# Kernel tuning notes

Hardware: AMD Instinct MI355X
Metric: run time of the kernel (lower is better)

The kernel has to match this reference:

```python
import jax, jax.numpy as jnp
import numpy as np

D_MODEL = 1024
NUM_HEADS = 16
D_K = D_MODEL // NUM_HEADS
THETA = 10000.0
SEQ = 2048
BATCH = 2


def _rope(t, positions):
    # t: [b, h, s, d_k]; positions: [s]
    half = D_K // 2
    freqs = 1.0 / (THETA ** (jnp.arange(0, D_K, 2, dtype=jnp.float32) / D_K))  # [half]
    angles = positions.astype(jnp.float32)[:, None] * freqs[None, :]  # [s, half]
    cos = jnp.cos(angles)  # [s, half]
    sin = jnp.sin(angles)
    tr = t.reshape(t.shape[:-1] + (half, 2))  # pairs are (even, odd) interleaved
    x1, x2 = tr[..., 0], tr[..., 1]
    r1 = x1 * cos - x2 * sin
    r2 = x1 * sin + x2 * cos
    return jnp.stack([r1, r2], axis=-1).reshape(t.shape)


def setup_inputs() -> dict:
    key = jax.random.key(0)
    ks = jax.random.split(key, 5)
    std = float(np.sqrt(2.0 / (D_MODEL + D_MODEL)))
    return {
        "x": jax.random.normal(ks[0], (BATCH, SEQ, D_MODEL), dtype=jnp.float32),
        "token_positions": jnp.arange(SEQ, dtype=jnp.int64 if jax.config.jax_enable_x64 else jnp.int32),
        "wq": std * jax.random.normal(ks[1], (D_MODEL, D_MODEL), dtype=jnp.float32),
        "wk": std * jax.random.normal(ks[2], (D_MODEL, D_MODEL), dtype=jnp.float32),
        "wv": std * jax.random.normal(ks[3], (D_MODEL, D_MODEL), dtype=jnp.float32),
        "wo": std * jax.random.normal(ks[4], (D_MODEL, D_MODEL), dtype=jnp.float32),
    }


def reference(x, token_positions, wq, wk, wv, wo):
    b, s, _ = x.shape
    # projections: weight is (d_out, d_in), y = x @ W^T
    def proj(w):
        y = jnp.einsum('bsd,od->bso', x, w)
        return y.reshape(b, s, NUM_HEADS, D_K).transpose(0, 2, 1, 3)  # [b,h,s,dk]
    Q, K, V = proj(wq), proj(wk), proj(wv)
    Q = _rope(Q, token_positions)
    K = _rope(K, token_positions)
    scale = 1.0 / jnp.sqrt(jnp.asarray(D_K, dtype=x.dtype))
    scores = jnp.einsum('bhqd,bhkd->bhqk', Q, K) * scale  # [b,h,s,s]
    causal = jnp.tril(jnp.ones((s, s), dtype=bool))
    scores = jnp.where(causal, scores, jnp.asarray(-jnp.inf, dtype=scores.dtype))
    attn = jax.nn.softmax(scores, axis=-1)
    out = jnp.einsum('bhqk,bhkd->bhqd', attn, V)  # [b,h,s,dk]
    out = out.transpose(0, 2, 1, 3).reshape(b, s, D_MODEL)
    return jnp.einsum('bsd,od->bso', out, wo)
```

## Files before the change

### kernel.cpp

```cpp
#include <hip/hip_runtime.h>
#include <hip/hip_bf16.h>
#include <math.h>

#define BATCH  2
#define SEQ    2048
#define DMODEL 1024
#define NHEADS 16
#define DK     64

typedef __hip_bfloat16 bf16;
typedef short s16x8 __attribute__((ext_vector_type(8)));
typedef float f32x4 __attribute__((ext_vector_type(4)));

union P8 { int4 i4; s16x8 v; short s[8]; };

static __device__ __forceinline__ unsigned short f2bu(float f) {
    bf16 h = __float2bfloat16(f);
    return *reinterpret_cast<unsigned short*>(&h);
}

static __device__ __forceinline__ void gll16(const void* g, void* l) {
    __builtin_amdgcn_global_load_lds(
        (const __attribute__((address_space(1))) unsigned int*)g,
        (__attribute__((address_space(3))) unsigned int*)l, 16, 0, 0);
}

#define BAR()    __builtin_amdgcn_s_barrier()
#define LGKM0()  do { asm volatile("s_waitcnt lgkmcnt(0)" ::: "memory"); \
                      __builtin_amdgcn_sched_barrier(0); } while (0)
#define WVM(n)   do { asm volatile("s_waitcnt vmcnt(" #n ")" ::: "memory"); \
                      __builtin_amdgcn_sched_barrier(0); } while (0)

__global__ __launch_bounds__(256) void conv_k(
    const float* __restrict__ x, const float* __restrict__ wq,
    const float* __restrict__ wk, const float* __restrict__ wv,
    const float* __restrict__ wo, bf16* __restrict__ dst)
{
    const size_t e0 = ((size_t)blockIdx.x * 256 + threadIdx.x) << 3;
    const float* src;
    bf16* d;
    if (e0 < (size_t)4194304) { src = x + e0; d = dst + e0; }
    else {
        const size_t r = e0 - 4194304;
        const int wsel = (int)(r >> 20);
        const size_t off = r & 1048575;
        src = (wsel == 0 ? wq : wsel == 1 ? wk : wsel == 2 ? wv : wo) + off;
        d = dst + 4194304 + ((size_t)wsel << 20) + off;
    }
    const float4 a = *(const float4*)src;
    const float4 b = *(const float4*)(src + 4);
    P8 p;
    p.s[0] = (short)f2bu(a.x); p.s[1] = (short)f2bu(a.y);
    p.s[2] = (short)f2bu(a.z); p.s[3] = (short)f2bu(a.w);
    p.s[4] = (short)f2bu(b.x); p.s[5] = (short)f2bu(b.y);
    p.s[6] = (short)f2bu(b.z); p.s[7] = (short)f2bu(b.w);
    *(int4*)d = p.i4;
}

__global__ __launch_bounds__(512, 2) void gemm_qkv(
    const bf16* __restrict__ Ab, const bf16* __restrict__ Wb,
    bf16* __restrict__ O0, bf16* __restrict__ O1, bf16* __restrict__ O2)
{
    __shared__ __align__(16) short As[2][256 * 64];
    __shared__ __align__(16) short Ws[2][256 * 64];
    const int tid  = threadIdx.x;
    const int wid  = tid >> 6;
    const int lane = tid & 63;
    const int ln   = lane & 15;
    const int quad = lane >> 4;
    const int wr   = wid >> 2;
    const int wc   = wid & 3;
    const int swz  = ln & 7;

    const int orig = blockIdx.x;
    const int wg = (orig & 7) * 24 + (orig >> 3);
    const int m_base = (wg & 15) << 8;
    const int nz = wg >> 4;
    const int z  = nz >> 2;
    const int n_base = (nz & 3) << 8;
    const bf16* Wz = Wb + ((size_t)z << 20);

    const int lrw = lane >> 3;
    const int lcs = ((lane & 7) ^ lrw) << 3;

    auto stageHalf = [&](int b, int kt, int q) {
        if (kt >= 16) return;
        const int rs = (q & 1) * 128 + wid * 16;
        if (q < 2) {
            const size_t src = (size_t)(m_base + rs + lrw) * DMODEL
                             + (size_t)(kt * 64 + lcs);
            short* d = &As[b][rs * 64];
            gll16(Ab + src,              d);
            gll16(Ab + src + 8 * DMODEL, d + 8 * 64);
        } else {
            const size_t src = (size_t)(n_base + rs + lrw) * DMODEL
                             + (size_t)(kt * 64 + lcs);
            short* d = &Ws[b][rs * 64];
            gll16(Wz + src,              d);
            gll16(Wz + src + 8 * DMODEL, d + 8 * 64);
        }
    };

    const f32x4 zero4 = {0.f, 0.f, 0.f, 0.f};
    f32x4 acc[8][4];
    #pragma unroll
    for (int i = 0; i < 8; ++i)
        #pragma unroll
        for (int j = 0; j < 4; ++j) acc[i][j] = zero4;

    s16x8 af[4][2], bw01[2][2], bw23[2][2];

    auto readA = [&](const short* Sb, int mg) {
        #pragma unroll
        for (int mi = 0; mi < 4; ++mi)
            #pragma unroll
            for (int kk = 0; kk < 2; ++kk)
                af[mi][kk] = *(const s16x8*)&Sb[
                    (wr * 128 + mg * 64 + 16 * mi + ln) * 64 +
                    ((((kk << 2) + quad) ^ swz) << 3)];
    };
    auto readB = [&](const short* Sb, int np, s16x8 (&bwp)[2][2]) {
        #pragma unroll
        for (int nj = 0; nj < 2; ++nj)
            #pragma unroll
            for (int kk = 0; kk < 2; ++kk)
                bwp[nj][kk] = *(const s16x8*)&Sb[
                    (wc * 64 + np * 32 + 16 * nj + ln) * 64 +
                    ((((kk << 2) + quad) ^ swz) << 3)];
    };
    auto mmac = [&](int mg, int np, const s16x8 (&bwp)[2][2]) {
        #pragma unroll
        for (int mi = 0; mi < 4; ++mi)
            #pragma unroll
            for (int nj = 0; nj < 2; ++nj)
                #pragma unroll
                for (int kk = 0; kk < 2; ++kk)
                    acc[mg * 4 + mi][np * 2 + nj] =
                        __builtin_amdgcn_mfma_f32_16x16x32_bf16(
                            af[mi][kk], bwp[nj][kk],
                            acc[mg * 4 + mi][np * 2 + nj], 0, 0, 0);
    };

    stageHalf(0, 0, 0); stageHalf(0, 0, 1);
    stageHalf(0, 0, 2); stageHalf(0, 0, 3);
    stageHalf(1, 1, 0);
    WVM(2);
    BAR();

    #pragma unroll 1
    for (int i = 0; i < 8; ++i) {
        const int ta = 2 * i, tb = 2 * i + 1;
        readA(As[0], 0); readB(Ws[0], 0, bw01);
        stageHalf(1, tb, 1);
        BAR(); LGKM0();
        __builtin_amdgcn_s_setprio(1); mmac(0, 0, bw01);
        __builtin_amdgcn_s_setprio(0); BAR();
        readB(Ws[0], 1, bw23);
        stageHalf(1, tb, 2);
        BAR(); LGKM0();
        __builtin_amdgcn_s_setprio(1); mmac(0, 1, bw23);
        __builtin_amdgcn_s_setprio(0); BAR();
        readA(As[0], 1);
        stageHalf(1, tb, 3);
        BAR(); LGKM0();
        __builtin_amdgcn_s_setprio(1); mmac(1, 0, bw01);
        __builtin_amdgcn_s_setprio(0); BAR();
        stageHalf(0, ta + 2, 0);
        if (i < 7) { WVM(2); } else { WVM(0); }
        BAR();
        __builtin_amdgcn_s_setprio(1); mmac(1, 1, bw23);
        __builtin_amdgcn_s_setprio(0); BAR();
        readA(As[1], 0); readB(Ws[1], 0, bw01);
        stageHalf(0, ta + 2, 1);
        BAR(); LGKM0();
        __builtin_amdgcn_s_setprio(1); mmac(0, 0, bw01);
        __builtin_amdgcn_s_setprio(0); BAR();
        readB(Ws[1], 1, bw23);
        stageHalf(0, ta + 2, 2);
        BAR(); LGKM0();
        __builtin_amdgcn_s_setprio(1); mmac(0, 1, bw23);
        __builtin_amdgcn_s_setprio(0); BAR();
        readA(As[1], 1);
        stageHalf(0, ta + 2, 3);
        BAR(); LGKM0();
        __builtin_amdgcn_s_setprio(1); mmac(1, 0, bw01);
        __builtin_amdgcn_s_setprio(0); BAR();
        stageHalf(1, tb + 2, 0);
        if (i < 7) { WVM(2); } else { WVM(0); }
        BAR();
        __builtin_amdgcn_s_setprio(1); mmac(1, 1, bw23);
        __builtin_amdgcn_s_setprio(0); BAR();
    }

    if (z < 2) {
        bf16* C = (z == 0) ? O0 : O1;
        const float qs = (z == 0) ? 0.125f * 1.44269504089f : 1.0f;
        const int h = (n_base >> 6) + wc;
        const float sgn = (ln & 1) ? 1.0f : -1.0f;
        float freq[4];
        #pragma unroll
        for (int nj = 0; nj < 4; ++nj)
            freq[nj] = exp2f(-(float)((16 * nj + ln) >> 1) * 0.4152410119f);
        #pragma unroll
        for (int mi = 0; mi < 8; ++mi) {
            #pragma unroll
            for (int r = 0; r < 4; ++r) {
                const int m = m_base + wr * 128 + 16 * mi + quad * 4 + r;
                const int b = m >> 11, s = m & (SEQ - 1);
                const float fs = (float)s;
                float sn[4], cs[4];
                #pragma unroll
                for (int nj = 0; nj < 4; ++nj)
                    __sincosf(fs * freq[nj], &sn[nj], &cs[nj]);
                bf16* row = C + (((size_t)(b * NHEADS + h) * SEQ) + s) * DK;
                #pragma unroll
                for (int nj = 0; nj < 4; ++nj) {
                    const float v = acc[mi][nj][r];
                    const float p = __shfl_xor(v, 1, 64);
                    row[16 * nj + ln] =
                        __float2bfloat16((v * cs[nj] + sgn * p * sn[nj]) * qs);
                }
            }
        }
    } else {
        #pragma unroll
        for (int nj = 0; nj < 4; ++nj) {
            const int n = n_base + wc * 64 + 16 * nj + ln;
            const int h = n >> 6, d = n & (DK - 1);
            #pragma unroll
            for (int mi = 0; mi < 8; ++mi) {
                const int m0v = m_base + wr * 128 + 16 * mi + quad * 4;
                const int b = m0v >> 11, s0 = m0v & (SEQ - 1);
                ushort4 pk;
                pk.x = f2bu(acc[mi][nj][0]); pk.y = f2bu(acc[mi][nj][1]);
                pk.z = f2bu(acc[mi][nj][2]); pk.w = f2bu(acc[mi][nj][3]);
                *(ushort4*)(O2 + (((size_t)(b * NHEADS + h) * DK) + d) * SEQ + s0) = pk;
            }
        }
    }
}

__global__ __launch_bounds__(256) void gemm_wo(
    const bf16* __restrict__ Ab, const bf16* __restrict__ Wb,
    float* __restrict__ Of)
{
    __shared__ __align__(16) short As[64 * 64];
    __shared__ __align__(16) short Ws2[128 * 64];
    const int tid  = threadIdx.x;
    const int w    = tid >> 6;
    const int lane = tid & 63;
    const int ln   = lane & 15;
    const int quad = lane >> 4;
    const int id   = blockIdx.x;
    const int m_base = (id & 63) << 6;
    const int n_base = (id >> 6) << 7;

    const int lrw = lane >> 3;
    const int lcs = ((lane & 7) ^ lrw) << 3;
    const int am = m_base + 16 * w + lrw;
    short* ldsA = &As[1024 * w];
    const size_t wbase = (size_t)(n_base + 32 * w + lrw) * DMODEL + lcs;
    short* ldsW = &Ws2[2048 * w];

    const f32x4 zero4 = {0.f, 0.f, 0.f, 0.f};
    f32x4 acc[2][4];
    #pragma unroll
    for (int i = 0; i < 2; ++i)
        #pragma unroll
        for (int j = 0; j < 4; ++j) acc[i][j] = zero4;

    const int mo = (w >> 1) << 5, no = (w & 1) << 6;
    const int swz = ln & 7;

    for (int k0 = 0; k0 < DMODEL; k0 += 64) {
        const int hh = k0 >> 6;
        __syncthreads();
        #pragma unroll
        for (int t = 0; t < 2; ++t) {
            const int m = am + t * 8;
            const int b = m >> 11, s = m & (SEQ - 1);
            gll16(Ab + (((size_t)(b * NHEADS + hh) * SEQ) + s) * DK + lcs,
                  ldsA + t * 512);
        }
        #pragma unroll
        for (int t = 0; t < 4; ++t)
            gll16(Wb + wbase + (size_t)t * 8 * DMODEL + k0, ldsW + t * 512);
        __syncthreads();
        #pragma unroll
        for (int t = 0; t < 2; ++t) {
            const int co = (((t << 2) + quad) ^ swz) << 3;
            s16x8 af[2], bw[4];
            #pragma unroll
            for (int i = 0; i < 2; ++i)
                af[i] = *(const s16x8*)&As[(mo + 16 * i + ln) * 64 + co];
            #pragma unroll
            for (int j = 0; j < 4; ++j)
                bw[j] = *(const s16x8*)&Ws2[(no + 16 * j + ln) * 64 + co];
            #pragma unroll
            for (int mi = 0; mi < 2; ++mi)
                #pragma unroll
                for (int ni = 0; ni < 4; ++ni)
                    acc[mi][ni] = __builtin_amdgcn_mfma_f32_16x16x32_bf16(
                        af[mi], bw[ni], acc[mi][ni], 0, 0, 0);
        }
    }

    #pragma unroll
    for (int mi = 0; mi < 2; ++mi)
        #pragma unroll
        for (int ni = 0; ni < 4; ++ni) {
            const int n = n_base + no + 16 * ni + ln;
            #pragma unroll
            for (int r = 0; r < 4; ++r) {
                const int m = m_base + mo + 16 * mi + quad * 4 + r;
                Of[(size_t)m * DMODEL + n] = acc[mi][ni][r];
            }
        }
}

__global__ __launch_bounds__(256) void attn_k(bf16* __restrict__ Q,
                                              const bf16* __restrict__ Kg,
                                              const bf16* __restrict__ VT)
{
    __shared__ __align__(16) short Ks[64 * 64];
    __shared__ __align__(16) short Vs[64 * 64];
    __shared__ __align__(16) short PT[4 * 16 * 64];
    const int tid  = threadIdx.x;
    const int w    = tid >> 6;
    const int lane = tid & 63;
    const int ln   = lane & 15;
    const int quad = lane >> 4;
    const int bh = blockIdx.x & 31;
    const int row = blockIdx.x >> 5;
    const int bk = row & 7, bg = row >> 3;
    const int qt = (bg == 0) ? 31 - bk : (bg == 1) ? 15 - bk
                 : (bg == 2) ? 16 + bk : bk;
    const size_t base = (size_t)bh * (SEQ * DK);
    const int srow = tid >> 2;
    const int sc   = (tid & 3) << 4;
    const int qrow = qt * 64 + 16 * w + ln;

    const int sr7 = srow & 7;
    const int wofs0 = srow * 64 + ((((sc >> 3)    ) ^ sr7) << 3);
    const int wofs1 = srow * 64 + ((((sc >> 3) | 1) ^ sr7) << 3);
    const int l7 = ln & 7;
    const int rof0 = ln * 64 + ((quad ^ l7) << 3);
    const int rof1 = ln * 64 + (((4 | quad) ^ l7) << 3);
    short* PTw = &PT[w << 10];

    P8 qa0, qa1;
    {
        const bf16* qsrc = Q + base + (size_t)qrow * DK + quad * 8;
        qa0.i4 = *(const int4*)(qsrc);
        qa1.i4 = *(const int4*)(qsrc + 32);
    }
    const f32x4 zero4 = {0.f, 0.f, 0.f, 0.f};
    f32x4 o[4];
    #pragma unroll
    for (int mt = 0; mt < 4; ++mt) o[mt] = zero4;
    float lsum = 0.f;

    P8 kk[2], vv[2];
    {
        const bf16* ksrc = Kg + base + (size_t)srow * DK + sc;
        kk[0].i4 = *(const int4*)(ksrc);
        kk[1].i4 = *(const int4*)(ksrc + 8);
        const bf16* vsrc = VT + base + (size_t)srow * SEQ + sc;
        vv[0].i4 = *(const int4*)(vsrc);
        vv[1].i4 = *(const int4*)(vsrc + 8);
    }

    for (int kb = 0; kb <= qt; ++kb) {
        __syncthreads();
        *(s16x8*)&Ks[wofs0] = kk[0].v;
        *(s16x8*)&Ks[wofs1] = kk[1].v;
        *(s16x8*)&Vs[wofs0] = vv[0].v;
        *(s16x8*)&Vs[wofs1] = vv[1].v;
        __syncthreads();

        if (kb < qt) {
            const bf16* ksrc = Kg + base + (size_t)((kb + 1) * 64 + srow) * DK + sc;
            kk[0].i4 = *(const int4*)(ksrc);
            kk[1].i4 = *(const int4*)(ksrc + 8);
            const bf16* vsrc = VT + base + (size_t)srow * SEQ + (kb + 1) * 64 + sc;
            vv[0].i4 = *(const int4*)(vsrc);
            vv[1].i4 = *(const int4*)(vsrc + 8);
        }

        f32x4 sf[4];
        #pragma unroll
        for (int mt = 0; mt < 4; ++mt) {
            sf[mt] = zero4;
            s16x8 ka  = *(const s16x8*)&Ks[mt * 1024 + rof0];
            s16x8 kb2 = *(const s16x8*)&Ks[mt * 1024 + rof1];
            sf[mt] = __builtin_amdgcn_mfma_f32_16x16x32_bf16(ka,  qa0.v, sf[mt], 0, 0, 0);
            sf[mt] = __builtin_amdgcn_mfma_f32_16x16x32_bf16(kb2, qa1.v, sf[mt], 0, 0, 0);
        }

        if (kb == qt) {
            #pragma unroll
            for (int mt = 0; mt < 4; ++mt)
                #pragma unroll
                for (int r = 0; r < 4; ++r)
                    if (kb * 64 + 16 * mt + quad * 4 + r > qrow) sf[mt][r] = -INFINITY;
        }
        #pragma unroll
        for (int mt = 0; mt < 4; ++mt)
            #pragma unroll
            for (int r = 0; r < 4; ++r) {
                sf[mt][r] = exp2f(sf[mt][r]);
                lsum += sf[mt][r];
            }

        #pragma unroll
        for (int mt = 0; mt < 4; ++mt) {
            ushort4 pk;
            pk.x = f2bu(sf[mt][0]); pk.y = f2bu(sf[mt][1]);
            pk.z = f2bu(sf[mt][2]); pk.w = f2bu(sf[mt][3]);
            *(ushort4*)&PTw[ln * 64 + ((((2 * mt) | (quad >> 1)) ^ l7) << 3)
                            + ((quad & 1) << 2)] = pk;
        }

        s16x8 pa0 = *(const s16x8*)&PTw[rof0];
        s16x8 pa1 = *(const s16x8*)&PTw[rof1];
        #pragma unroll
        for (int mt = 0; mt < 4; ++mt) {
            s16x8 va0 = *(const s16x8*)&Vs[mt * 1024 + rof0];
            s16x8 va1 = *(const s16x8*)&Vs[mt * 1024 + rof1];
            o[mt] = __builtin_amdgcn_mfma_f32_16x16x32_bf16(va0, pa0, o[mt], 0, 0, 0);
            o[mt] = __builtin_amdgcn_mfma_f32_16x16x32_bf16(va1, pa1, o[mt], 0, 0, 0);
        }
    }

    lsum += __shfl_xor(lsum, 16, 64);
    lsum += __shfl_xor(lsum, 32, 64);
    const float inv = 1.0f / lsum;
    #pragma unroll
    for (int mt = 0; mt < 4; ++mt) {
        ushort4 st;
        st.x = f2bu(o[mt][0] * inv); st.y = f2bu(o[mt][1] * inv);
        st.z = f2bu(o[mt][2] * inv); st.w = f2bu(o[mt][3] * inv);
        *(ushort4*)(Q + base + (size_t)qrow * DK + 16 * mt + quad * 4) = st;
    }
}

extern "C" void kernel_launch(void* const* d_in, const int* in_sizes, int n_in,
                              void* d_out, int out_size, void* d_ws, size_t ws_size,
                              hipStream_t stream)
{
    const float* x  = (const float*)d_in[0];
    const float* wq = (const float*)d_in[2];
    const float* wk = (const float*)d_in[3];
    const float* wv = (const float*)d_in[4];
    const float* wo = (const float*)d_in[5];

    bf16* wsb   = (bf16*)d_ws;
    bf16* xb    = wsb;
    bf16* wqkvb = wsb + ((size_t)4 << 20);
    bf16* wob   = wsb + ((size_t)7 << 20);
    bf16* Qw    = wsb + ((size_t)8 << 20);
    bf16* Kw    = wsb + ((size_t)12 << 20);
    bf16* VTw   = wsb + ((size_t)16 << 20);

    conv_k<<<4096, 256, 0, stream>>>(x, wq, wk, wv, wo, wsb);
    gemm_qkv<<<192, 512, 0, stream>>>(xb, wqkvb, Qw, Kw, VTw);
    attn_k<<<1024, 256, 0, stream>>>(Qw, Kw, VTw);
    gemm_wo<<<512, 256, 0, stream>>>(Qw, wob, (float*)d_out);
}
```

Baseline: 174.7 us.

## Enlarge gemm_wo tile to 128x128 and stage whole tiles in QKV GEMM

```diff
diff --git a/kernel.cpp b/kernel.cpp
--- a/kernel.cpp
+++ b/kernel.cpp
@@ -100,6 +100,10 @@
             gll16(Wz + src + 8 * DMODEL, d + 8 * 64);
         }
     };
+    auto stageTile = [&](int b, int kt) {
+        stageHalf(b, kt, 0); stageHalf(b, kt, 1);
+        stageHalf(b, kt, 2); stageHalf(b, kt, 3);
+    };
 
     const f32x4 zero4 = {0.f, 0.f, 0.f, 0.f};
     f32x4 acc[8][4];
@@ -141,52 +145,45 @@
                             acc[mg * 4 + mi][np * 2 + nj], 0, 0, 0);
     };
 
-    stageHalf(0, 0, 0); stageHalf(0, 0, 1);
-    stageHalf(0, 0, 2); stageHalf(0, 0, 3);
-    stageHalf(1, 1, 0);
-    WVM(2);
+    stageTile(0, 0);
+    stageTile(1, 1);
+    WVM(8);
     BAR();
 
     #pragma unroll 1
     for (int i = 0; i < 8; ++i) {
         const int ta = 2 * i, tb = 2 * i + 1;
         readA(As[0], 0); readB(Ws[0], 0, bw01);
-        stageHalf(1, tb, 1);
         BAR(); LGKM0();
         __builtin_amdgcn_s_setprio(1); mmac(0, 0, bw01);
         __builtin_amdgcn_s_setprio(0); BAR();
         readB(Ws[0], 1, bw23);
-        stageHalf(1, tb, 2);
         BAR(); LGKM0();
         __builtin_amdgcn_s_setprio(1); mmac(0, 1, bw23);
         __builtin_amdgcn_s_setprio(0); BAR();
         readA(As[0], 1);
-        stageHalf(1, tb, 3);
         BAR(); LGKM0();
         __builtin_amdgcn_s_setprio(1); mmac(1, 0, bw01);
         __builtin_amdgcn_s_setprio(0); BAR();
-        stageHalf(0, ta + 2, 0);
-        if (i < 7) { WVM(2); } else { WVM(0); }
+        stageTile(0, ta + 2);
+        if (i < 7) { WVM(8); } else { WVM(0); }
         BAR();
         __builtin_amdgcn_s_setprio(1); mmac(1, 1, bw23);
         __builtin_amdgcn_s_setprio(0); BAR();
         readA(As[1], 0); readB(Ws[1], 0, bw01);
-        stageHalf(0, ta + 2, 1);
         BAR(); LGKM0();
         __builtin_amdgcn_s_setprio(1); mmac(0, 0, bw01);
         __builtin_amdgcn_s_setprio(0); BAR();
         readB(Ws[1], 1, bw23);
-        stageHalf(0, ta + 2, 2);
         BAR(); LGKM0();
         __builtin_amdgcn_s_setprio(1); mmac(0, 1, bw23);
         __builtin_amdgcn_s_setprio(0); BAR();
         readA(As[1], 1);
-        stageHalf(0, ta + 2, 3);
         BAR(); LGKM0();
         __builtin_amdgcn_s_setprio(1); mmac(1, 0, bw01);
         __builtin_amdgcn_s_setprio(0); BAR();
-        stageHalf(1, tb + 2, 0);
-        if (i < 7) { WVM(2); } else { WVM(0); }
+        stageTile(1, tb + 2);
+        if (i < 7) { WVM(8); } else { WVM(0); }
         BAR();
         __builtin_amdgcn_s_setprio(1); mmac(1, 1, bw23);
         __builtin_amdgcn_s_setprio(0); BAR();
@@ -244,7 +241,7 @@
     const bf16* __restrict__ Ab, const bf16* __restrict__ Wb,
     float* __restrict__ Of)
 {
-    __shared__ __align__(16) short As[64 * 64];
+    __shared__ __align__(16) short As[128 * 64];
     __shared__ __align__(16) short Ws2[128 * 64];
     const int tid  = threadIdx.x;
     const int w    = tid >> 6;
@@ -252,52 +249,48 @@
     const int ln   = lane & 15;
     const int quad = lane >> 4;
     const int id   = blockIdx.x;
-    const int m_base = (id & 63) << 6;
-    const int n_base = (id >> 6) << 7;
+    const int m_base = (id & 31) << 7;
+    const int n_base = (id >> 5) << 7;
 
     const int lrw = lane >> 3;
     const int lcs = ((lane & 7) ^ lrw) << 3;
-    const int am = m_base + 16 * w + lrw;
-    short* ldsA = &As[1024 * w];
+    short* ldsA = &As[2048 * w];
+    short* ldsW = &Ws2[2048 * w];
     const size_t wbase = (size_t)(n_base + 32 * w + lrw) * DMODEL + lcs;
-    short* ldsW = &Ws2[2048 * w];
 
     const f32x4 zero4 = {0.f, 0.f, 0.f, 0.f};
-    f32x4 acc[2][4];
+    f32x4 acc[4][4];
     #pragma unroll
-    for (int i = 0; i < 2; ++i)
+    for (int i = 0; i < 4; ++i)
         #pragma unroll
         for (int j = 0; j < 4; ++j) acc[i][j] = zero4;
 
-    const int mo = (w >> 1) << 5, no = (w & 1) << 6;
+    const int mo = (w >> 1) << 6, no = (w & 1) << 6;
     const int swz = ln & 7;
 
     for (int k0 = 0; k0 < DMODEL; k0 += 64) {
         const int hh = k0 >> 6;
         __syncthreads();
         #pragma unroll
-        for (int t = 0; t < 2; ++t) {
-            const int m = am + t * 8;
+        for (int t = 0; t < 4; ++t) {
+            const int m = m_base + 32 * w + 8 * t + lrw;
             const int b = m >> 11, s = m & (SEQ - 1);
             gll16(Ab + (((size_t)(b * NHEADS + hh) * SEQ) + s) * DK + lcs,
                   ldsA + t * 512);
-        }
-        #pragma unroll
-        for (int t = 0; t < 4; ++t)
             gll16(Wb + wbase + (size_t)t * 8 * DMODEL + k0, ldsW + t * 512);
+        }
         __syncthreads();
         #pragma unroll
         for (int t = 0; t < 2; ++t) {
             const int co = (((t << 2) + quad) ^ swz) << 3;
-            s16x8 af[2], bw[4];
-            #pragma unroll
-            for (int i = 0; i < 2; ++i)
+            s16x8 af[4], bw[4];
+            #pragma unroll
+            for (int i = 0; i < 4; ++i) {
                 af[i] = *(const s16x8*)&As[(mo + 16 * i + ln) * 64 + co];
-            #pragma unroll
-            for (int j = 0; j < 4; ++j)
-                bw[j] = *(const s16x8*)&Ws2[(no + 16 * j + ln) * 64 + co];
-            #pragma unroll
-            for (int mi = 0; mi < 2; ++mi)
+                bw[i] = *(const s16x8*)&Ws2[(no + 16 * i + ln) * 64 + co];
+            }
+            #pragma unroll
+            for (int mi = 0; mi < 4; ++mi)
                 #pragma unroll
                 for (int ni = 0; ni < 4; ++ni)
                     acc[mi][ni] = __builtin_amdgcn_mfma_f32_16x16x32_bf16(
@@ -306,7 +299,7 @@
     }
 
     #pragma unroll
-    for (int mi = 0; mi < 2; ++mi)
+    for (int mi = 0; mi < 4; ++mi)
         #pragma unroll
         for (int ni = 0; ni < 4; ++ni) {
             const int n = n_base + no + 16 * ni + ln;
@@ -465,5 +458,5 @@
     conv_k<<<4096, 256, 0, stream>>>(x, wq, wk, wv, wo, wsb);
     gemm_qkv<<<192, 512, 0, stream>>>(xb, wqkvb, Qw, Kw, VTw);
     attn_k<<<1024, 256, 0, stream>>>(Qw, Kw, VTw);
-    gemm_wo<<<512, 256, 0, stream>>>(Qw, wob, (float*)d_out);
-}
+    gemm_wo<<<256, 256, 0, stream>>>(Qw, wob, (float*)d_out);
+}
```

Result: slower. 180.8 us (+3.5%).

## Split long causal query tiles across two KV halves and add combine kernel

Applied to the files above, without the earlier changes.

```diff
diff --git a/kernel.cpp b/kernel.cpp
--- a/kernel.cpp
+++ b/kernel.cpp
@@ -320,7 +320,9 @@
 
 __global__ __launch_bounds__(256) void attn_k(bf16* __restrict__ Q,
                                               const bf16* __restrict__ Kg,
-                                              const bf16* __restrict__ VT)
+                                              const bf16* __restrict__ VT,
+                                              float* __restrict__ Opart,
+                                              float* __restrict__ Lpart)
 {
     __shared__ __align__(16) short Ks[64 * 64];
     __shared__ __align__(16) short Vs[64 * 64];
@@ -330,11 +332,21 @@
     const int lane = tid & 63;
     const int ln   = lane & 15;
     const int quad = lane >> 4;
-    const int bh = blockIdx.x & 31;
-    const int row = blockIdx.x >> 5;
-    const int bk = row & 7, bg = row >> 3;
-    const int qt = (bg == 0) ? 31 - bk : (bg == 1) ? 15 - bk
-                 : (bg == 2) ? 16 + bk : bk;
+    const int bh   = blockIdx.x & 31;
+    const int slot = blockIdx.x >> 5;
+    int qt, kb0, kb1, half;
+    bool split;
+    if (slot < 32) {
+        qt   = 31 - (slot >> 1);
+        half = slot & 1;
+        const int nt = qt + 1, h0 = nt >> 1;
+        kb0 = half ? h0 : 0;
+        kb1 = half ? nt : h0;
+        split = true;
+    } else {
+        qt = 15 - (slot - 32);
+        kb0 = 0; kb1 = qt + 1; half = 0; split = false;
+    }
     const size_t base = (size_t)bh * (SEQ * DK);
     const int srow = tid >> 2;
     const int sc   = (tid & 3) << 4;
@@ -362,15 +374,15 @@
 
     P8 kk[2], vv[2];
     {
-        const bf16* ksrc = Kg + base + (size_t)srow * DK + sc;
+        const bf16* ksrc = Kg + base + (size_t)(kb0 * 64 + srow) * DK + sc;
         kk[0].i4 = *(const int4*)(ksrc);
         kk[1].i4 = *(const int4*)(ksrc + 8);
-        const bf16* vsrc = VT + base + (size_t)srow * SEQ + sc;
+        const bf16* vsrc = VT + base + (size_t)srow * SEQ + kb0 * 64 + sc;
         vv[0].i4 = *(const int4*)(vsrc);
         vv[1].i4 = *(const int4*)(vsrc + 8);
     }
 
-    for (int kb = 0; kb <= qt; ++kb) {
+    for (int kb = kb0; kb < kb1; ++kb) {
         __syncthreads();
         *(s16x8*)&Ks[wofs0] = kk[0].v;
         *(s16x8*)&Ks[wofs1] = kk[1].v;
@@ -378,7 +390,7 @@
         *(s16x8*)&Vs[wofs1] = vv[1].v;
         __syncthreads();
 
-        if (kb < qt) {
+        if (kb + 1 < kb1) {
             const bf16* ksrc = Kg + base + (size_t)((kb + 1) * 64 + srow) * DK + sc;
             kk[0].i4 = *(const int4*)(ksrc);
             kk[1].i4 = *(const int4*)(ksrc + 8);
@@ -434,14 +446,52 @@
 
     lsum += __shfl_xor(lsum, 16, 64);
     lsum += __shfl_xor(lsum, 32, 64);
-    const float inv = 1.0f / lsum;
-    #pragma unroll
-    for (int mt = 0; mt < 4; ++mt) {
-        ushort4 st;
-        st.x = f2bu(o[mt][0] * inv); st.y = f2bu(o[mt][1] * inv);
-        st.z = f2bu(o[mt][2] * inv); st.w = f2bu(o[mt][3] * inv);
-        *(ushort4*)(Q + base + (size_t)qrow * DK + 16 * mt + quad * 4) = st;
-    }
+
+    if (split) {
+        const size_t tb = ((size_t)(bh * 16 + (qt - 16)) * 2 + half);
+        float* Opw = Opart + tb * 4096 + (size_t)(16 * w + ln) * 64;
+        #pragma unroll
+        for (int mt = 0; mt < 4; ++mt) {
+            float4 st = make_float4(o[mt][0], o[mt][1], o[mt][2], o[mt][3]);
+            *(float4*)&Opw[16 * mt + quad * 4] = st;
+        }
+        if (quad == 0) Lpart[tb * 64 + 16 * w + ln] = lsum;
+    } else {
+        const float inv = 1.0f / lsum;
+        #pragma unroll
+        for (int mt = 0; mt < 4; ++mt) {
+            ushort4 st;
+            st.x = f2bu(o[mt][0] * inv); st.y = f2bu(o[mt][1] * inv);
+            st.z = f2bu(o[mt][2] * inv); st.w = f2bu(o[mt][3] * inv);
+            *(ushort4*)(Q + base + (size_t)qrow * DK + 16 * mt + quad * 4) = st;
+        }
+    }
+}
+
+__global__ __launch_bounds__(256) void attn_combine(
+    const float* __restrict__ Opart, const float* __restrict__ Lpart,
+    bf16* __restrict__ Q)
+{
+    const int e   = blockIdx.x * 256 + threadIdx.x;
+    const int c0  = (e & 7) << 3;
+    const int row = (e >> 3) & 63;
+    const int qtb = (e >> 9) & 15;
+    const int bh  = e >> 13;
+    const size_t tb = (size_t)(bh * 16 + qtb) * 2;
+    const size_t b0 = tb * 4096 + (size_t)row * 64 + c0;
+    const float4 a0 = *(const float4*)&Opart[b0];
+    const float4 a1 = *(const float4*)&Opart[b0 + 4];
+    const float4 c0v = *(const float4*)&Opart[b0 + 4096];
+    const float4 c1v = *(const float4*)&Opart[b0 + 4100];
+    const float inv = 1.0f / (Lpart[tb * 64 + row] + Lpart[tb * 64 + 64 + row]);
+    ushort4 s0, s1;
+    s0.x = f2bu((a0.x + c0v.x) * inv); s0.y = f2bu((a0.y + c0v.y) * inv);
+    s0.z = f2bu((a0.z + c0v.z) * inv); s0.w = f2bu((a0.w + c0v.w) * inv);
+    s1.x = f2bu((a1.x + c1v.x) * inv); s1.y = f2bu((a1.y + c1v.y) * inv);
+    s1.z = f2bu((a1.z + c1v.z) * inv); s1.w = f2bu((a1.w + c1v.w) * inv);
+    bf16* dst = Q + ((size_t)bh * SEQ + (16 + qtb) * 64 + row) * DK + c0;
+    *(ushort4*)dst = s0;
+    *(ushort4*)(dst + 4) = s1;
 }
 
 extern "C" void kernel_launch(void* const* d_in, const int* in_sizes, int n_in,
@@ -461,9 +511,12 @@
     bf16* Qw    = wsb + ((size_t)8 << 20);
     bf16* Kw    = wsb + ((size_t)12 << 20);
     bf16* VTw   = wsb + ((size_t)16 << 20);
+    float* Opart = (float*)((char*)d_ws + ((size_t)40 << 20));
+    float* Lpart = (float*)((char*)d_ws + ((size_t)56 << 20));
 
     conv_k<<<4096, 256, 0, stream>>>(x, wq, wk, wv, wo, wsb);
     gemm_qkv<<<192, 512, 0, stream>>>(xb, wqkvb, Qw, Kw, VTw);
-    attn_k<<<1024, 256, 0, stream>>>(Qw, Kw, VTw);
+    attn_k<<<1536, 256, 0, stream>>>(Qw, Kw, VTw, Opart, Lpart);
+    attn_combine<<<1024, 256, 0, stream>>>(Opart, Lpart, Qw);
     gemm_wo<<<512, 256, 0, stream>>>(Qw, wob, (float*)d_out);
 }
```

Result: slower. 179.0 us (+2.5%).

## Stage 128-key super-tiles in attention to halve barrier count per key range

Applied to the files above, without the earlier changes.

```diff
diff --git a/kernel.cpp b/kernel.cpp
--- a/kernel.cpp
+++ b/kernel.cpp
@@ -322,8 +322,8 @@
                                               const bf16* __restrict__ Kg,
                                               const bf16* __restrict__ VT)
 {
-    __shared__ __align__(16) short Ks[64 * 64];
-    __shared__ __align__(16) short Vs[64 * 64];
+    __shared__ __align__(16) short Ks[128 * 64];
+    __shared__ __align__(16) short Vs[64 * 128];
     __shared__ __align__(16) short PT[4 * 16 * 64];
     const int tid  = threadIdx.x;
     const int w    = tid >> 6;
@@ -336,16 +336,21 @@
     const int qt = (bg == 0) ? 31 - bk : (bg == 1) ? 15 - bk
                  : (bg == 2) ? 16 + bk : bk;
     const size_t base = (size_t)bh * (SEQ * DK);
-    const int srow = tid >> 2;
-    const int sc   = (tid & 3) << 4;
     const int qrow = qt * 64 + 16 * w + ln;
 
-    const int sr7 = srow & 7;
-    const int wofs0 = srow * 64 + ((((sc >> 3)    ) ^ sr7) << 3);
-    const int wofs1 = srow * 64 + ((((sc >> 3) | 1) ^ sr7) << 3);
+    const int srk = tid >> 1, sck = (tid & 1) << 5;
+    const int srv = tid >> 2, scv = (tid & 3) << 5;
+    int wK[4], wV[4];
+    #pragma unroll
+    for (int j = 0; j < 4; ++j) {
+        wK[j] = srk * 64  + ((((sck >> 3) + j) ^ (srk & 7)) << 3);
+        wV[j] = srv * 128 + ((((scv >> 3) + j) ^ (srv & 7)) << 3);
+    }
     const int l7 = ln & 7;
     const int rof0 = ln * 64 + ((quad ^ l7) << 3);
     const int rof1 = ln * 64 + (((4 | quad) ^ l7) << 3);
+    const int vr0 = ln * 128 + ((quad ^ l7) << 3);
+    const int vr1 = ln * 128 + (((4 | quad) ^ l7) << 3);
     short* PTw = &PT[w << 10];
 
     P8 qa0, qa1;
@@ -360,49 +365,40 @@
     for (int mt = 0; mt < 4; ++mt) o[mt] = zero4;
     float lsum = 0.f;
 
-    P8 kk[2], vv[2];
-    {
-        const bf16* ksrc = Kg + base + (size_t)srow * DK + sc;
+    P8 kk[4], vv[4];
+    auto loadSup = [&](int u) {
+        const bf16* ksrc = Kg + base + (size_t)(u * 128 + srk) * DK + sck;
         kk[0].i4 = *(const int4*)(ksrc);
         kk[1].i4 = *(const int4*)(ksrc + 8);
-        const bf16* vsrc = VT + base + (size_t)srow * SEQ + sc;
+        kk[2].i4 = *(const int4*)(ksrc + 16);
+        kk[3].i4 = *(const int4*)(ksrc + 24);
+        const bf16* vsrc = VT + base + (size_t)srv * SEQ + u * 128 + scv;
         vv[0].i4 = *(const int4*)(vsrc);
         vv[1].i4 = *(const int4*)(vsrc + 8);
-    }
-
-    for (int kb = 0; kb <= qt; ++kb) {
-        __syncthreads();
-        *(s16x8*)&Ks[wofs0] = kk[0].v;
-        *(s16x8*)&Ks[wofs1] = kk[1].v;
-        *(s16x8*)&Vs[wofs0] = vv[0].v;
-        *(s16x8*)&Vs[wofs1] = vv[1].v;
-        __syncthreads();
-
-        if (kb < qt) {
-            const bf16* ksrc = Kg + base + (size_t)((kb + 1) * 64 + srow) * DK + sc;
-            kk[0].i4 = *(const int4*)(ksrc);
-            kk[1].i4 = *(const int4*)(ksrc + 8);
-            const bf16* vsrc = VT + base + (size_t)srow * SEQ + (kb + 1) * 64 + sc;
-            vv[0].i4 = *(const int4*)(vsrc);
-            vv[1].i4 = *(const int4*)(vsrc + 8);
-        }
-
+        vv[2].i4 = *(const int4*)(vsrc + 16);
+        vv[3].i4 = *(const int4*)(vsrc + 24);
+    };
+
+    const int nt = qt + 1;
+    const int nsup = (nt + 1) >> 1;
+
+    auto subPhase = [&](int u, int s) {
+        const int t64 = 2 * u + s;
         f32x4 sf[4];
         #pragma unroll
         for (int mt = 0; mt < 4; ++mt) {
             sf[mt] = zero4;
-            s16x8 ka  = *(const s16x8*)&Ks[mt * 1024 + rof0];
-            s16x8 kb2 = *(const s16x8*)&Ks[mt * 1024 + rof1];
+            s16x8 ka  = *(const s16x8*)&Ks[s * 4096 + mt * 1024 + rof0];
+            s16x8 kb2 = *(const s16x8*)&Ks[s * 4096 + mt * 1024 + rof1];
             sf[mt] = __builtin_amdgcn_mfma_f32_16x16x32_bf16(ka,  qa0.v, sf[mt], 0, 0, 0);
             sf[mt] = __builtin_amdgcn_mfma_f32_16x16x32_bf16(kb2, qa1.v, sf[mt], 0, 0, 0);
         }
-
-        if (kb == qt) {
+        if (t64 == qt) {
             #pragma unroll
             for (int mt = 0; mt < 4; ++mt)
                 #pragma unroll
                 for (int r = 0; r < 4; ++r)
-                    if (kb * 64 + 16 * mt + quad * 4 + r > qrow) sf[mt][r] = -INFINITY;
+                    if (t64 * 64 + 16 * mt + quad * 4 + r > qrow) sf[mt][r] = -INFINITY;
         }
         #pragma unroll
         for (int mt = 0; mt < 4; ++mt)
@@ -411,7 +407,6 @@
                 sf[mt][r] = exp2f(sf[mt][r]);
                 lsum += sf[mt][r];
             }
-
         #pragma unroll
         for (int mt = 0; mt < 4; ++mt) {
             ushort4 pk;
@@ -420,16 +415,30 @@
             *(ushort4*)&PTw[ln * 64 + ((((2 * mt) | (quad >> 1)) ^ l7) << 3)
                             + ((quad & 1) << 2)] = pk;
         }
-
         s16x8 pa0 = *(const s16x8*)&PTw[rof0];
         s16x8 pa1 = *(const s16x8*)&PTw[rof1];
         #pragma unroll
         for (int mt = 0; mt < 4; ++mt) {
-            s16x8 va0 = *(const s16x8*)&Vs[mt * 1024 + rof0];
-            s16x8 va1 = *(const s16x8*)&Vs[mt * 1024 + rof1];
+            s16x8 va0 = *(const s16x8*)&Vs[mt * 2048 + s * 64 + vr0];
+            s16x8 va1 = *(const s16x8*)&Vs[mt * 2048 + s * 64 + vr1];
             o[mt] = __builtin_amdgcn_mfma_f32_16x16x32_bf16(va0, pa0, o[mt], 0, 0, 0);
             o[mt] = __builtin_amdgcn_mfma_f32_16x16x32_bf16(va1, pa1, o[mt], 0, 0, 0);
         }
+    };
+
+    loadSup(0);
+    #pragma unroll 1
+    for (int u = 0; u < nsup; ++u) {
+        __syncthreads();
+        #pragma unroll
+        for (int j = 0; j < 4; ++j) *(s16x8*)&Ks[wK[j]] = kk[j].v;
+        #pragma unroll
+        for (int j = 0; j < 4; ++j) *(s16x8*)&Vs[wV[j]] = vv[j].v;
+        __syncthreads();
+        if (u + 1 < nsup) loadSup(u + 1);
+
+        subPhase(u, 0);
+        if (2 * u + 1 < nt) subPhase(u, 1);
     }
 
     lsum += __shfl_xor(lsum, 16, 64);
```

New measurement: 174.6 us. Within noise of the previous version (-0.0%).
